# Kernel optimization log

Measured on AMD Instinct MI355X. Metric: run time of the kernel, lower is better.

## Reference

```python
import jax, jax.numpy as jnp
import numpy as np

U, I, D, L, NNZ, B = 100000, 50000, 64, 3, 3200000, 4096
N = U + I
MOMENTUM = 0.05

def setup_inputs() -> dict:
    key = jax.random.key(0)
    ks = jax.random.split(key, 10)
    return {
        'user_emb': jax.random.normal(ks[0], (U, D), jnp.float32) * 0.02,
        'item_emb': jax.random.normal(ks[1], (I, D), jnp.float32) * 0.02,
        'W': jax.random.normal(ks[2], (D, D), jnp.float32) * (1.0 / np.sqrt(D)),
        'b': jnp.zeros((D,), jnp.float32),
        'adj_rows': jax.random.randint(ks[3], (NNZ,), 0, N, jnp.int32),
        'adj_cols': jax.random.randint(ks[4], (NNZ,), 0, N, jnp.int32),
        'adj_vals': jax.random.uniform(ks[5], (NNZ,), jnp.float32) * 0.05,
        'users': jax.random.randint(ks[6], (B,), 0, U, jnp.int32),
        'items': jax.random.randint(ks[7], (B,), 0, I, jnp.int32),
        'u_his': jax.random.normal(ks[8], (U, D), jnp.float32),
        'i_his': jax.random.normal(ks[9], (I, D), jnp.float32),
    }

def _spmm(rows, cols, vals, x):
    # y = A @ x for sparse COO A: gather source rows, scale, scatter-add to dest rows
    return jax.ops.segment_sum(vals[:, None] * x[cols], rows, num_segments=N)

def reference(user_emb, item_emb, W, b, adj_rows, adj_cols, adj_vals, users, items, u_his, i_his):
    ego = jnp.concatenate([user_emb, item_emb], axis=0)  # [N, D]
    acc = ego
    cur = ego
    for _ in range(L):
        cur = _spmm(adj_rows, adj_cols, adj_vals, cur)
        acc = acc + cur
    all_emb = acc / (L + 1)           # mean over stacked layers
    u_all = all_emb[:U]
    i_all = all_emb[U:]
    u_online = u_all[users]           # [B, D]
    i_online = i_all[items]
    m = MOMENTUM
    u_target = jax.lax.stop_gradient(u_his[users] * m + u_online * (1.0 - m))
    i_target = jax.lax.stop_gradient(i_his[items] * m + i_online * (1.0 - m))
    p_u = u_online @ W.T + b
    p_i = i_online @ W.T + b
    return (p_u, u_target, p_i, i_target)
```

## Files before the change

### kernel.cpp

```cpp
#include <hip/hip_runtime.h>
#include <hip/hip_bf16.h>

#define U_CNT   100000
#define I_CNT   50000
#define D_DIM   64
#define N_NODES 150000
#define NNZ_E   3200000
#define B_SZ    4096

#define SUPER_SHIFT 12
#define NSUP 37
#define TILE1_E 4096
#define N_TILES1 ((NNZ_E + TILE1_E - 1) / TILE1_E)
#define TILE2_E 2048

#define CAP_SUP 98304
#define CAP2 4096
#define NSUB (NSUP * 32)
#define P2_BLOCKS_PER_SUP 24

#define CONV_THREADS (N_NODES * 16)
#define CONV_BLOCKS ((CONV_THREADS + 255) / 256)

typedef unsigned int uint;
typedef unsigned short ushort_t;
typedef _Float16 half_t;
typedef half_t half2_t __attribute__((ext_vector_type(2)));

union h2u_t { uint u; half2_t h; };
__device__ __forceinline__ half2_t u2h2(uint u) { h2u_t c; c.u = u; return c.h; }
__device__ __forceinline__ uint h22u(half2_t h) { h2u_t c; c.h = h; return c.u; }
__device__ __forceinline__ half2_t h2shfl_xor(half2_t v, int m) {
    h2u_t c; c.h = v; c.u = (uint)__shfl_xor((int)c.u, m, 64); return c.h;
}
__device__ __forceinline__ float h2lo(uint u) { return (float)u2h2(u)[0]; }
__device__ __forceinline__ float h2hi(uint u) { return (float)u2h2(u)[1]; }

__global__ __launch_bounds__(256) void init_cursors_kernel(int* __restrict__ scursor,
                                                           int* __restrict__ subcursor) {
    int i = blockIdx.x * 256 + threadIdx.x;
    if (i < NSUP) scursor[i] = i * CAP_SUP;
    if (i < NSUB) subcursor[i] = i * CAP2;
}

__global__ __launch_bounds__(256) void super_scatter_kernel(const int* __restrict__ rows,
                                                            const int* __restrict__ cols,
                                                            const float* __restrict__ vals,
                                                            int* __restrict__ scursor,
                                                            int2* __restrict__ smeta,
                                                            const float4* __restrict__ ue4,
                                                            const float4* __restrict__ ie4,
                                                            uint2* __restrict__ e2) {
    __shared__ int2 stage[TILE1_E];
    __shared__ int lcnt[NSUP];
    __shared__ int lbase[NSUP];
    __shared__ int gbase[NSUP];
    int tid = threadIdx.x;

    if (blockIdx.x >= N_TILES1) {
        int g = (blockIdx.x - N_TILES1) * 256 + tid;
        if (g < CONV_THREADS) {
            float4 f = (g < U_CNT * 16) ? ue4[g] : ie4[g - U_CNT * 16];
            half2_t a = { (half_t)f.x, (half_t)f.y };
            half2_t b = { (half_t)f.z, (half_t)f.w };
            uint2 o; o.x = h22u(a); o.y = h22u(b);
            e2[g] = o;
        }
        return;
    }

    int tile = blockIdx.x;
    int base = tile * TILE1_E;
    int cnt_tile = NNZ_E - base;
    if (cnt_tile > TILE1_E) cnt_tile = TILE1_E;

    if (tid < NSUP) lcnt[tid] = 0;
    __syncthreads();

    int nk = cnt_tile - tid;
    nk = (nk <= 0) ? 0 : (nk + 255) >> 8;

    int pk[16]; float vv[16]; int sp[16]; int rk[16];
    #pragma unroll
    for (int k = 0; k < 16; ++k) {
        if (k < nk) {
            int j = base + tid + (k << 8);
            int r = rows[j];
            int c = cols[j];
            vv[k] = vals[j];
            sp[k] = r >> SUPER_SHIFT;
            pk[k] = ((r & ((1 << SUPER_SHIFT) - 1)) << 18) | c;
            rk[k] = atomicAdd(&lcnt[sp[k]], 1);
        }
    }
    __syncthreads();

    if (tid < 64) {
        int c = (tid < NSUP) ? lcnt[tid] : 0;
        int incl = c;
        #pragma unroll
        for (int off = 1; off < 64; off <<= 1) {
            int t = __shfl_up(incl, off, 64);
            if (tid >= off) incl += t;
        }
        if (tid < NSUP) {
            lbase[tid] = incl - c;
            gbase[tid] = atomicAdd(&scursor[tid], c);
        }
    }
    __syncthreads();

    #pragma unroll
    for (int k = 0; k < 16; ++k) {
        if (k < nk) stage[lbase[sp[k]] + rk[k]] = make_int2(pk[k], __float_as_int(vv[k]));
    }
    __syncthreads();

    int wv = tid >> 6, ln = tid & 63;
    for (int s = wv; s < NSUP; s += 4) {
        int c = lcnt[s], lb = lbase[s], gb = gbase[s];
        int lim = (s + 1) * CAP_SUP;
        for (int t = ln; t < c; t += 64)
            if (gb + t < lim) smeta[gb + t] = stage[lb + t];
    }
}

__global__ __launch_bounds__(256) void sub_scatter_kernel(const int2* __restrict__ smeta,
                                                          const int* __restrict__ scursor,
                                                          int* __restrict__ subcursor,
                                                          int2* __restrict__ meta) {
    __shared__ int2 stage[TILE2_E];
    __shared__ int lcnt[32];
    __shared__ int lbase[32];
    __shared__ int gbase[32];
    int tid = threadIdx.x;
    int s    = blockIdx.x / P2_BLOCKS_PER_SUP;
    int slot = blockIdx.x % P2_BLOCKS_PER_SUP;
    int beg = s * CAP_SUP;
    int cnt_s = scursor[s] - beg;
    if (cnt_s > CAP_SUP) cnt_s = CAP_SUP;
    int end = beg + cnt_s;

    for (int tb = beg + slot * TILE2_E; tb < end; tb += P2_BLOCKS_PER_SUP * TILE2_E) {
        int cnt_tile = end - tb;
        if (cnt_tile > TILE2_E) cnt_tile = TILE2_E;

        if (tid < 32) lcnt[tid] = 0;
        __syncthreads();

        int nk = cnt_tile - tid;
        nk = (nk <= 0) ? 0 : (nk + 255) >> 8;

        int2 ed[8]; int sb[8]; int rk[8];
        #pragma unroll
        for (int k = 0; k < 8; ++k) {
            if (k < nk) {
                ed[k] = smeta[tb + tid + (k << 8)];
                sb[k] = ((uint)ed[k].x >> 25) & 31;
                rk[k] = atomicAdd(&lcnt[sb[k]], 1);
            }
        }
        __syncthreads();

        if (tid < 64) {
            int c = (tid < 32) ? lcnt[tid] : 0;
            int incl = c;
            #pragma unroll
            for (int off = 1; off < 32; off <<= 1) {
                int t = __shfl_up(incl, off, 64);
                if (tid >= off) incl += t;
            }
            if (tid < 32) {
                lbase[tid] = incl - c;
                gbase[tid] = atomicAdd(&subcursor[(s << 5) + tid], c);
            }
        }
        __syncthreads();

        #pragma unroll
        for (int k = 0; k < 8; ++k) {
            if (k < nk) stage[lbase[sb[k]] + rk[k]] = ed[k];
        }
        __syncthreads();

        int wv = tid >> 6, ln = tid & 63;
        for (int b = wv; b < 32; b += 4) {
            int c = lcnt[b], lb = lbase[b], gb = gbase[b];
            int lim = ((s << 5) + b + 1) * CAP2;
            for (int t = ln; t < c; t += 64)
                if (gb + t < lim) meta[gb + t] = stage[lb + t];
        }
        __syncthreads();
    }
}

__global__ __launch_bounds__(256) void row_sort_kernel(const int* __restrict__ subcursor,
                                                       int2* __restrict__ meta,
                                                       int* __restrict__ rstart,
                                                       int* __restrict__ rend) {
    __shared__ int2 stage[CAP2];
    __shared__ int rcnt[128];
    __shared__ int scan[128];
    __shared__ int cur[128];
    int g = blockIdx.x;
    int base = g * CAP2;
    int cnt = subcursor[g] - base;
    if (cnt > CAP2) cnt = CAP2;
    int tid = threadIdx.x;
    int s = g >> 5, q = g & 31;
    int r0 = (s << SUPER_SHIFT) + (q << 7);

    if (tid < 128) rcnt[tid] = 0;
    __syncthreads();

    for (int i = tid; i < cnt; i += 256) {
        int2 e = meta[base + i];
        stage[i] = e;
        atomicAdd(&rcnt[((uint)e.x >> 18) & 127], 1);
    }
    __syncthreads();

    if (tid < 128) scan[tid] = rcnt[tid];
    __syncthreads();
    for (int off = 1; off < 128; off <<= 1) {
        int t = (tid < 128 && tid >= off) ? scan[tid - off] : 0;
        __syncthreads();
        if (tid < 128) scan[tid] += t;
        __syncthreads();
    }
    if (tid < 128) {
        int excl = scan[tid] - rcnt[tid];
        cur[tid] = excl;
        int r = r0 + tid;
        if (r < N_NODES) {
            rstart[r] = base + excl;
            rend[r]   = base + scan[tid];
        }
    }
    __syncthreads();

    for (int i = tid; i < cnt; i += 256) {
        int2 e = stage[i];
        int rl = ((uint)e.x >> 18) & 127;
        int pos = atomicAdd(&cur[rl], 1);
        float v = __int_as_float(e.y);
        half2_t hv = { (half_t)v, (half_t)v };
        meta[base + pos] = make_int2(e.x & 0x3FFFF, (int)h22u(hv));
    }
}

__global__ __launch_bounds__(256) void spmm_fp16_kernel(const int* __restrict__ rstart,
                                                        const int* __restrict__ rend,
                                                        const int2* __restrict__ csr,
                                                        const ushort_t* __restrict__ x,
                                                        ushort_t* __restrict__ out) {
    int wid  = (blockIdx.x * blockDim.x + threadIdx.x) >> 6;
    int lane = threadIdx.x & 63;
    int sub  = lane >> 3;
    int l8   = lane & 7;
    if (wid >= N_NODES) return;
    int s = rstart[wid], e = rend[wid];
    const uint4* x4 = (const uint4*)x;

    int last = e - 1; if (last < s) last = s;
    auto ld = [&](int jj) -> int2 {
        int2 c = csr[jj < e ? jj : last];
        if (jj >= e) c.y = 0;
        return c;
    };

    half2_t a0 = { (half_t)0, (half_t)0 };
    half2_t a1 = a0, a2 = a0, a3 = a0;

    int j = s + sub;
    int2 c0 = ld(j);
    int2 c1 = ld(j + 8);
    int2 c2 = ld(j + 16);
    int2 c3 = ld(j + 24);
    for (; j < e; j += 32) {
        uint4 x0 = x4[(size_t)(c0.x & 0x3FFFF) * 8 + l8];
        uint4 x1 = x4[(size_t)(c1.x & 0x3FFFF) * 8 + l8];
        uint4 x2 = x4[(size_t)(c2.x & 0x3FFFF) * 8 + l8];
        uint4 x3 = x4[(size_t)(c3.x & 0x3FFFF) * 8 + l8];
        int jn = j + 32;
        int2 n0 = ld(jn);
        int2 n1 = ld(jn + 8);
        int2 n2 = ld(jn + 16);
        int2 n3 = ld(jn + 24);
        half2_t v0 = u2h2((uint)c0.y);
        a0 += u2h2(x0.x) * v0; a1 += u2h2(x0.y) * v0;
        a2 += u2h2(x0.z) * v0; a3 += u2h2(x0.w) * v0;
        half2_t v1 = u2h2((uint)c1.y);
        a0 += u2h2(x1.x) * v1; a1 += u2h2(x1.y) * v1;
        a2 += u2h2(x1.z) * v1; a3 += u2h2(x1.w) * v1;
        half2_t v2 = u2h2((uint)c2.y);
        a0 += u2h2(x2.x) * v2; a1 += u2h2(x2.y) * v2;
        a2 += u2h2(x2.z) * v2; a3 += u2h2(x2.w) * v2;
        half2_t v3 = u2h2((uint)c3.y);
        a0 += u2h2(x3.x) * v3; a1 += u2h2(x3.y) * v3;
        a2 += u2h2(x3.z) * v3; a3 += u2h2(x3.w) * v3;
        c0 = n0; c1 = n1; c2 = n2; c3 = n3;
    }
    a0 += h2shfl_xor(a0, 8);  a1 += h2shfl_xor(a1, 8);
    a2 += h2shfl_xor(a2, 8);  a3 += h2shfl_xor(a3, 8);
    a0 += h2shfl_xor(a0, 16); a1 += h2shfl_xor(a1, 16);
    a2 += h2shfl_xor(a2, 16); a3 += h2shfl_xor(a3, 16);
    a0 += h2shfl_xor(a0, 32); a1 += h2shfl_xor(a1, 32);
    a2 += h2shfl_xor(a2, 32); a3 += h2shfl_xor(a3, 32);

    if (sub == 0) {
        uint4 r;
        r.x = h22u(a0); r.y = h22u(a1); r.z = h22u(a2); r.w = h22u(a3);
        ((uint4*)out)[(size_t)wid * 8 + l8] = r;
    }
}

__global__ __launch_bounds__(256) void epilogue_kernel(const int* __restrict__ users,
                                                       const int* __restrict__ items,
                                                       const int* __restrict__ rstart,
                                                       const int* __restrict__ rend,
                                                       const int2* __restrict__ csr,
                                                       const ushort_t* __restrict__ ebuf,
                                                       const ushort_t* __restrict__ buf1,
                                                       const ushort_t* __restrict__ buf2,
                                                       const float* __restrict__ u_his,
                                                       const float* __restrict__ i_his,
                                                       const float* __restrict__ W,
                                                       const float* __restrict__ bvec,
                                                       float* __restrict__ out) {
    __shared__ float Wt[D_DIM * 65];
    __shared__ float bsh[D_DIM];
    __shared__ float on_s[4][D_DIM];
    for (int t = threadIdx.x; t < D_DIM * D_DIM; t += blockDim.x) {
        int j = t >> 6, k = t & 63;
        Wt[k * 65 + j] = W[t];
    }
    if (threadIdx.x < D_DIM) bsh[threadIdx.x] = bvec[threadIdx.x];

    int wv   = threadIdx.x >> 6;
    int wid  = blockIdx.x * 4 + wv;
    int lane = threadIdx.x & 63;
    int sub  = lane >> 4;
    int l16  = lane & 15;

    bool is_user = (wid < B_SZ);
    int  samp = is_user ? wid : wid - B_SZ;
    int  idx  = is_user ? users[samp] : items[samp];
    int  row  = is_user ? idx : (U_CNT + idx);

    const float* his = is_user ? u_his : i_his;
    float hisv = his[(size_t)idx * D_DIM + lane];
    uint2 eg = make_uint2(0, 0), b1v = eg, b2v = eg;
    if (sub == 0) {
        eg  = ((const uint2*)ebuf)[(size_t)row * 16 + l16];
        b1v = ((const uint2*)buf1)[(size_t)row * 16 + l16];
        b2v = ((const uint2*)buf2)[(size_t)row * 16 + l16];
    }

    int s = rstart[row], e = rend[row];
    int last = e - 1; if (last < s) last = s;
    auto ld = [&](int jj) -> int2 {
        int2 c = csr[jj < e ? jj : last];
        if (jj >= e) c.y = 0;
        return c;
    };
    half2_t c0 = { (half_t)0, (half_t)0 };
    half2_t c1 = c0;
    int j = s + sub;
    int2 e0 = ld(j);
    int2 e1 = ld(j + 4);
    int2 e2 = ld(j + 8);
    int2 e3 = ld(j + 12);
    for (; j < e; j += 16) {
        uint2 x0 = ((const uint2*)buf2)[(size_t)(e0.x & 0x3FFFF) * 16 + l16];
        uint2 x1 = ((const uint2*)buf2)[(size_t)(e1.x & 0x3FFFF) * 16 + l16];
        uint2 x2 = ((const uint2*)buf2)[(size_t)(e2.x & 0x3FFFF) * 16 + l16];
        uint2 x3 = ((const uint2*)buf2)[(size_t)(e3.x & 0x3FFFF) * 16 + l16];
        int jn = j + 16;
        int2 n0 = ld(jn);
        int2 n1 = ld(jn + 4);
        int2 n2 = ld(jn + 8);
        int2 n3 = ld(jn + 12);
        half2_t v0 = u2h2((uint)e0.y);
        c0 += u2h2(x0.x) * v0; c1 += u2h2(x0.y) * v0;
        half2_t v1 = u2h2((uint)e1.y);
        c0 += u2h2(x1.x) * v1; c1 += u2h2(x1.y) * v1;
        half2_t v2 = u2h2((uint)e2.y);
        c0 += u2h2(x2.x) * v2; c1 += u2h2(x2.y) * v2;
        half2_t v3 = u2h2((uint)e3.y);
        c0 += u2h2(x3.x) * v3; c1 += u2h2(x3.y) * v3;
        e0 = n0; e1 = n1; e2 = n2; e3 = n3;
    }
    c0 += h2shfl_xor(c0, 16); c1 += h2shfl_xor(c1, 16);
    c0 += h2shfl_xor(c0, 32); c1 += h2shfl_xor(c1, 32);

    if (sub == 0) {
        on_s[wv][l16 * 4 + 0] = (h2lo(eg.x) + h2lo(b1v.x) + h2lo(b2v.x) + (float)c0[0]) * 0.25f;
        on_s[wv][l16 * 4 + 1] = (h2hi(eg.x) + h2hi(b1v.x) + h2hi(b2v.x) + (float)c0[1]) * 0.25f;
        on_s[wv][l16 * 4 + 2] = (h2lo(eg.y) + h2lo(b1v.y) + h2lo(b2v.y) + (float)c1[0]) * 0.25f;
        on_s[wv][l16 * 4 + 3] = (h2hi(eg.y) + h2hi(b1v.y) + h2hi(b2v.y) + (float)c1[1]) * 0.25f;
    }
    __syncthreads();

    float online = on_s[wv][lane];
    float target = 0.05f * hisv + 0.95f * online;

    float p = bsh[lane];
    #pragma unroll
    for (int k = 0; k < D_DIM; ++k) {
        float ok = __shfl(online, k, 64);
        p = fmaf(ok, Wt[k * 65 + lane], p);
    }

    size_t base = is_user ? 0 : (size_t)2 * B_SZ * D_DIM;
    out[base + (size_t)samp * D_DIM + lane] = p;
    out[base + (size_t)B_SZ * D_DIM + (size_t)samp * D_DIM + lane] = target;
}


extern "C" void kernel_launch(void* const* d_in, const int* in_sizes, int n_in,
                              void* d_out, int out_size, void* d_ws, size_t ws_size,
                              hipStream_t stream) {
    const float* user_emb = (const float*)d_in[0];
    const float* item_emb = (const float*)d_in[1];
    const float* W        = (const float*)d_in[2];
    const float* bvec     = (const float*)d_in[3];
    const int*   adj_rows = (const int*)d_in[4];
    const int*   adj_cols = (const int*)d_in[5];
    const float* adj_vals = (const float*)d_in[6];
    const int*   users    = (const int*)d_in[7];
    const int*   items    = (const int*)d_in[8];
    const float* u_his    = (const float*)d_in[9];
    const float* i_his    = (const float*)d_in[10];
    float* out = (float*)d_out;

    char* ws = (char*)d_ws;
    size_t o = 0;
    ushort_t* ebuf  = (ushort_t*)(ws + o); o += (size_t)N_NODES * D_DIM * 2;
    ushort_t* buf1  = (ushort_t*)(ws + o); o += (size_t)N_NODES * D_DIM * 2;
    int2*  smeta    = (int2*)(ws + o);     o += (size_t)NSUP * CAP_SUP * 8;
    int2*  meta     = (int2*)(ws + o);     o += (size_t)NSUB * CAP2 * 8;
    int*   rstart   = (int*)(ws + o);      o += (size_t)N_NODES * 4;
    int*   rend     = (int*)(ws + o);      o += (size_t)N_NODES * 4;
    int*   scursor  = (int*)(ws + o);      o += 64 * 4;
    int*   subcursor= (int*)(ws + o);      o += (size_t)NSUB * 4;
    ushort_t* buf2  = (ushort_t*)smeta;
    (void)ws_size; (void)o; (void)in_sizes; (void)n_in; (void)out_size;

    init_cursors_kernel<<<(NSUB + 255) / 256, 256, 0, stream>>>(scursor, subcursor);
    super_scatter_kernel<<<N_TILES1 + CONV_BLOCKS, 256, 0, stream>>>(
        adj_rows, adj_cols, adj_vals, scursor, smeta,
        (const float4*)user_emb, (const float4*)item_emb, (uint2*)ebuf);
    sub_scatter_kernel<<<NSUP * P2_BLOCKS_PER_SUP, 256, 0, stream>>>(smeta, scursor,
                                                                     subcursor, meta);
    row_sort_kernel<<<NSUB, 256, 0, stream>>>(subcursor, meta, rstart, rend);

    int spmm_blocks = (N_NODES + 3) / 4;
    spmm_fp16_kernel<<<spmm_blocks, 256, 0, stream>>>(rstart, rend, meta, ebuf, buf1);
    spmm_fp16_kernel<<<spmm_blocks, 256, 0, stream>>>(rstart, rend, meta, buf1, buf2);

    epilogue_kernel<<<(2 * B_SZ) / 4, 256, 0, stream>>>(users, items, rstart, rend, meta,
                                                        ebuf, buf1, buf2,
                                                        u_his, i_his, W, bvec, out);
}
```

Before: 332.7 us.

## Fuse row sort into first SpMM layer and stage CSR segments in shared memory

Merges the per-bucket row sort with the first SpMM pass. Each 512-thread block sorts its 128-row bucket in registers and shared memory, using a wave shuffle scan, then computes those rows directly from the LDS-staged edge list. The second layer reloads the bucket's edges into LDS and reuses them the same way. This removes one kernel launch and the global re-read of the CSR metadata. In exchange, each block now handles a fixed 128 rows with 8 waves of 16 rows each, so rows with many edges can leave the load unbalanced, and there are far fewer blocks than before (1184 versus 37500).

New measurement: 328.7 us. About the same (-1.2%).

```diff
diff --git a/kernel.cpp b/kernel.cpp
--- a/kernel.cpp
+++ b/kernel.cpp
@@ -194,124 +194,142 @@
     }
 }
 
-__global__ __launch_bounds__(256) void row_sort_kernel(const int* __restrict__ subcursor,
-                                                       int2* __restrict__ meta,
-                                                       int* __restrict__ rstart,
-                                                       int* __restrict__ rend) {
+template<int SORT>
+__global__ __launch_bounds__(512) void sort_spmm_kernel(const int* __restrict__ subcursor,
+                                                        int2* __restrict__ meta,
+                                                        int* __restrict__ rstart,
+                                                        int* __restrict__ rend,
+                                                        const ushort_t* __restrict__ x,
+                                                        ushort_t* __restrict__ out) {
     __shared__ int2 stage[CAP2];
     __shared__ int rcnt[128];
-    __shared__ int scan[128];
-    __shared__ int cur[128];
+    __shared__ int rs[128];
+    __shared__ int re_[128];
     int g = blockIdx.x;
     int base = g * CAP2;
     int cnt = subcursor[g] - base;
     if (cnt > CAP2) cnt = CAP2;
     int tid = threadIdx.x;
-    int s = g >> 5, q = g & 31;
-    int r0 = (s << SUPER_SHIFT) + (q << 7);
-
-    if (tid < 128) rcnt[tid] = 0;
-    __syncthreads();
-
-    for (int i = tid; i < cnt; i += 256) {
-        int2 e = meta[base + i];
-        stage[i] = e;
-        atomicAdd(&rcnt[((uint)e.x >> 18) & 127], 1);
-    }
-    __syncthreads();
-
-    if (tid < 128) scan[tid] = rcnt[tid];
-    __syncthreads();
-    for (int off = 1; off < 128; off <<= 1) {
-        int t = (tid < 128 && tid >= off) ? scan[tid - off] : 0;
-        __syncthreads();
-        if (tid < 128) scan[tid] += t;
-        __syncthreads();
-    }
-    if (tid < 128) {
-        int excl = scan[tid] - rcnt[tid];
-        cur[tid] = excl;
-        int r = r0 + tid;
-        if (r < N_NODES) {
-            rstart[r] = base + excl;
-            rend[r]   = base + scan[tid];
-        }
-    }
-    __syncthreads();
-
-    for (int i = tid; i < cnt; i += 256) {
-        int2 e = stage[i];
-        int rl = ((uint)e.x >> 18) & 127;
-        int pos = atomicAdd(&cur[rl], 1);
-        float v = __int_as_float(e.y);
-        half2_t hv = { (half_t)v, (half_t)v };
-        meta[base + pos] = make_int2(e.x & 0x3FFFF, (int)h22u(hv));
-    }
-}
-
-__global__ __launch_bounds__(256) void spmm_fp16_kernel(const int* __restrict__ rstart,
-                                                        const int* __restrict__ rend,
-                                                        const int2* __restrict__ csr,
-                                                        const ushort_t* __restrict__ x,
-                                                        ushort_t* __restrict__ out) {
-    int wid  = (blockIdx.x * blockDim.x + threadIdx.x) >> 6;
-    int lane = threadIdx.x & 63;
+    int r0 = ((g >> 5) << SUPER_SHIFT) + ((g & 31) << 7);
+
+    if (SORT) {
+        if (tid < 128) rcnt[tid] = 0;
+        __syncthreads();
+
+        int2 ek[8]; int rk[8];
+        int nk = cnt - tid;
+        nk = (nk <= 0) ? 0 : (nk + 511) >> 9;
+        #pragma unroll
+        for (int k = 0; k < 8; ++k) {
+            if (k < nk) {
+                ek[k] = meta[base + tid + (k << 9)];
+                rk[k] = atomicAdd(&rcnt[((uint)ek[k].x >> 18) & 127], 1);
+            }
+        }
+        __syncthreads();
+
+        if (tid < 64) {
+            int c0 = rcnt[2 * tid], c1 = rcnt[2 * tid + 1];
+            int s2 = c0 + c1, incl = s2;
+            #pragma unroll
+            for (int off = 1; off < 64; off <<= 1) {
+                int t = __shfl_up(incl, off, 64);
+                if (tid >= off) incl += t;
+            }
+            int s0 = incl - s2, s1 = incl - c1;
+            rs[2 * tid] = s0;      re_[2 * tid] = s0 + c0;
+            rs[2 * tid + 1] = s1;  re_[2 * tid + 1] = incl;
+            int r = r0 + 2 * tid;
+            if (r < N_NODES)     { rstart[r]     = base + s0; rend[r]     = base + s0 + c0; }
+            if (r + 1 < N_NODES) { rstart[r + 1] = base + s1; rend[r + 1] = base + incl;    }
+        }
+        __syncthreads();
+
+        #pragma unroll
+        for (int k = 0; k < 8; ++k) {
+            if (k < nk) {
+                int rl = ((uint)ek[k].x >> 18) & 127;
+                int pos = rs[rl] + rk[k];
+                float v = __int_as_float(ek[k].y);
+                half2_t hv = { (half_t)v, (half_t)v };
+                int2 f = make_int2(ek[k].x & 0x3FFFF, (int)h22u(hv));
+                stage[pos] = f;
+                meta[base + pos] = f;
+            }
+        }
+        __syncthreads();
+    } else {
+        for (int i = tid; i < cnt; i += 512) stage[i] = meta[base + i];
+        if (tid < 128) {
+            int r = r0 + tid;
+            if (r < N_NODES) { rs[tid] = rstart[r] - base; re_[tid] = rend[r] - base; }
+            else             { rs[tid] = 0; re_[tid] = 0; }
+        }
+        __syncthreads();
+    }
+
+    int wv   = tid >> 6;
+    int lane = tid & 63;
     int sub  = lane >> 3;
     int l8   = lane & 7;
-    if (wid >= N_NODES) return;
-    int s = rstart[wid], e = rend[wid];
     const uint4* x4 = (const uint4*)x;
 
-    int last = e - 1; if (last < s) last = s;
-    auto ld = [&](int jj) -> int2 {
-        int2 c = csr[jj < e ? jj : last];
-        if (jj >= e) c.y = 0;
-        return c;
-    };
-
-    half2_t a0 = { (half_t)0, (half_t)0 };
-    half2_t a1 = a0, a2 = a0, a3 = a0;
-
-    int j = s + sub;
-    int2 c0 = ld(j);
-    int2 c1 = ld(j + 8);
-    int2 c2 = ld(j + 16);
-    int2 c3 = ld(j + 24);
-    for (; j < e; j += 32) {
-        uint4 x0 = x4[(size_t)(c0.x & 0x3FFFF) * 8 + l8];
-        uint4 x1 = x4[(size_t)(c1.x & 0x3FFFF) * 8 + l8];
-        uint4 x2 = x4[(size_t)(c2.x & 0x3FFFF) * 8 + l8];
-        uint4 x3 = x4[(size_t)(c3.x & 0x3FFFF) * 8 + l8];
-        int jn = j + 32;
-        int2 n0 = ld(jn);
-        int2 n1 = ld(jn + 8);
-        int2 n2 = ld(jn + 16);
-        int2 n3 = ld(jn + 24);
-        half2_t v0 = u2h2((uint)c0.y);
-        a0 += u2h2(x0.x) * v0; a1 += u2h2(x0.y) * v0;
-        a2 += u2h2(x0.z) * v0; a3 += u2h2(x0.w) * v0;
-        half2_t v1 = u2h2((uint)c1.y);
-        a0 += u2h2(x1.x) * v1; a1 += u2h2(x1.y) * v1;
-        a2 += u2h2(x1.z) * v1; a3 += u2h2(x1.w) * v1;
-        half2_t v2 = u2h2((uint)c2.y);
-        a0 += u2h2(x2.x) * v2; a1 += u2h2(x2.y) * v2;
-        a2 += u2h2(x2.z) * v2; a3 += u2h2(x2.w) * v2;
-        half2_t v3 = u2h2((uint)c3.y);
-        a0 += u2h2(x3.x) * v3; a1 += u2h2(x3.y) * v3;
-        a2 += u2h2(x3.z) * v3; a3 += u2h2(x3.w) * v3;
-        c0 = n0; c1 = n1; c2 = n2; c3 = n3;
-    }
-    a0 += h2shfl_xor(a0, 8);  a1 += h2shfl_xor(a1, 8);
-    a2 += h2shfl_xor(a2, 8);  a3 += h2shfl_xor(a3, 8);
-    a0 += h2shfl_xor(a0, 16); a1 += h2shfl_xor(a1, 16);
-    a2 += h2shfl_xor(a2, 16); a3 += h2shfl_xor(a3, 16);
-    a0 += h2shfl_xor(a0, 32); a1 += h2shfl_xor(a1, 32);
-    a2 += h2shfl_xor(a2, 32); a3 += h2shfl_xor(a3, 32);
-
-    if (sub == 0) {
-        uint4 r;
-        r.x = h22u(a0); r.y = h22u(a1); r.z = h22u(a2); r.w = h22u(a3);
-        ((uint4*)out)[(size_t)wid * 8 + l8] = r;
+    for (int rr = 0; rr < 16; ++rr) {
+        int rl = (wv << 4) + rr;
+        int s = rs[rl], e = re_[rl];
+        half2_t a0 = { (half_t)0, (half_t)0 };
+        half2_t a1 = a0, a2 = a0, a3 = a0;
+
+        if (e > s) {
+            int last = e - 1;
+            auto ldl = [&](int jj) -> int2 {
+                int2 c = stage[jj < e ? jj : last];
+                if (jj >= e) c.y = 0;
+                return c;
+            };
+            int j = s + sub;
+            int2 c0 = ldl(j);
+            int2 c1 = ldl(j + 8);
+            int2 c2 = ldl(j + 16);
+            int2 c3 = ldl(j + 24);
+            for (; j < e; j += 32) {
+                uint4 x0 = x4[(size_t)(c0.x & 0x3FFFF) * 8 + l8];
+                uint4 x1 = x4[(size_t)(c1.x & 0x3FFFF) * 8 + l8];
+                uint4 x2 = x4[(size_t)(c2.x & 0x3FFFF) * 8 + l8];
+                uint4 x3 = x4[(size_t)(c3.x & 0x3FFFF) * 8 + l8];
+                int jn = j + 32;
+                int2 n0 = ldl(jn);
+                int2 n1 = ldl(jn + 8);
+                int2 n2 = ldl(jn + 16);
+                int2 n3 = ldl(jn + 24);
+                half2_t v0 = u2h2((uint)c0.y);
+                a0 += u2h2(x0.x) * v0; a1 += u2h2(x0.y) * v0;
+                a2 += u2h2(x0.z) * v0; a3 += u2h2(x0.w) * v0;
+                half2_t v1 = u2h2((uint)c1.y);
+                a0 += u2h2(x1.x) * v1; a1 += u2h2(x1.y) * v1;
+                a2 += u2h2(x1.z) * v1; a3 += u2h2(x1.w) * v1;
+                half2_t v2 = u2h2((uint)c2.y);
+                a0 += u2h2(x2.x) * v2; a1 += u2h2(x2.y) * v2;
+                a2 += u2h2(x2.z) * v2; a3 += u2h2(x2.w) * v2;
+                half2_t v3 = u2h2((uint)c3.y);
+                a0 += u2h2(x3.x) * v3; a1 += u2h2(x3.y) * v3;
+                a2 += u2h2(x3.z) * v3; a3 += u2h2(x3.w) * v3;
+                c0 = n0; c1 = n1; c2 = n2; c3 = n3;
+            }
+        }
+        a0 += h2shfl_xor(a0, 8);  a1 += h2shfl_xor(a1, 8);
+        a2 += h2shfl_xor(a2, 8);  a3 += h2shfl_xor(a3, 8);
+        a0 += h2shfl_xor(a0, 16); a1 += h2shfl_xor(a1, 16);
+        a2 += h2shfl_xor(a2, 16); a3 += h2shfl_xor(a3, 16);
+        a0 += h2shfl_xor(a0, 32); a1 += h2shfl_xor(a1, 32);
+        a2 += h2shfl_xor(a2, 32); a3 += h2shfl_xor(a3, 32);
+
+        int wid = r0 + rl;
+        if (sub == 0 && wid < N_NODES) {
+            uint4 r;
+            r.x = h22u(a0); r.y = h22u(a1); r.z = h22u(a2); r.w = h22u(a3);
+            ((uint4*)out)[(size_t)wid * 8 + l8] = r;
+        }
     }
 }
 
@@ -453,11 +471,11 @@
         (const float4*)user_emb, (const float4*)item_emb, (uint2*)ebuf);
     sub_scatter_kernel<<<NSUP * P2_BLOCKS_PER_SUP, 256, 0, stream>>>(smeta, scursor,
                                                                      subcursor, meta);
-    row_sort_kernel<<<NSUB, 256, 0, stream>>>(subcursor, meta, rstart, rend);
-
-    int spmm_blocks = (N_NODES + 3) / 4;
-    spmm_fp16_kernel<<<spmm_blocks, 256, 0, stream>>>(rstart, rend, meta, ebuf, buf1);
-    spmm_fp16_kernel<<<spmm_blocks, 256, 0, stream>>>(rstart, rend, meta, buf1, buf2);
+
+    sort_spmm_kernel<1><<<NSUB, 512, 0, stream>>>(subcursor, meta, rstart, rend,
+                                                  ebuf, buf1);
+    sort_spmm_kernel<0><<<NSUB, 512, 0, stream>>>(subcursor, meta, rstart, rend,
+                                                  buf1, buf2);
 
     epilogue_kernel<<<(2 * B_SZ) / 4, 256, 0, stream>>>(users, items, rstart, rend, meta,
                                                         ebuf, buf1, buf2,
```

## Replace multi-pass bucket sort with direct per-row atomic slot scatter

Applied to the files above, without the earlier changes.

Drops the three-stage COO-to-CSR build (super-bucket scatter, sub-bucket scatter, per-row counting sort) in favour of one scatter kernel. That kernel reserves a slot in a fixed-capacity ELL-like region per destination row (56 slots) with a global atomicAdd and writes the column and fp16 value there. The SpMM and epilogue kernels then read each row from its fixed offset using the per-row cursor as its end. This removes two kernel launches and several full passes over the edge list. In exchange it relies on about 3.2M global atomics spread over 150k counters, uses a larger padded metadata buffer, and silently drops edges for any row with more than 56 entries. Edge order within a row is also no longer deterministic, so fp16 summation order can vary between runs.

Measured after the change: 490.8 us. +47.5%, slower.

```diff
diff --git a/kernel.cpp b/kernel.cpp
--- a/kernel.cpp
+++ b/kernel.cpp
@@ -8,16 +8,10 @@
 #define NNZ_E   3200000
 #define B_SZ    4096
 
-#define SUPER_SHIFT 12
-#define NSUP 37
 #define TILE1_E 4096
 #define N_TILES1 ((NNZ_E + TILE1_E - 1) / TILE1_E)
-#define TILE2_E 2048
-
-#define CAP_SUP 98304
-#define CAP2 4096
-#define NSUB (NSUP * 32)
-#define P2_BLOCKS_PER_SUP 24
+
+#define CAP_ROW 56
 
 #define CONV_THREADS (N_NODES * 16)
 #define CONV_BLOCKS ((CONV_THREADS + 255) / 256)
@@ -36,25 +30,19 @@
 __device__ __forceinline__ float h2lo(uint u) { return (float)u2h2(u)[0]; }
 __device__ __forceinline__ float h2hi(uint u) { return (float)u2h2(u)[1]; }
 
-__global__ __launch_bounds__(256) void init_cursors_kernel(int* __restrict__ scursor,
-                                                           int* __restrict__ subcursor) {
+__global__ __launch_bounds__(256) void init_rowcur_kernel(int* __restrict__ rowcur) {
     int i = blockIdx.x * 256 + threadIdx.x;
-    if (i < NSUP) scursor[i] = i * CAP_SUP;
-    if (i < NSUB) subcursor[i] = i * CAP2;
-}
-
-__global__ __launch_bounds__(256) void super_scatter_kernel(const int* __restrict__ rows,
-                                                            const int* __restrict__ cols,
-                                                            const float* __restrict__ vals,
-                                                            int* __restrict__ scursor,
-                                                            int2* __restrict__ smeta,
-                                                            const float4* __restrict__ ue4,
-                                                            const float4* __restrict__ ie4,
-                                                            uint2* __restrict__ e2) {
-    __shared__ int2 stage[TILE1_E];
-    __shared__ int lcnt[NSUP];
-    __shared__ int lbase[NSUP];
-    __shared__ int gbase[NSUP];
+    if (i < N_NODES) rowcur[i] = i * CAP_ROW;
+}
+
+__global__ __launch_bounds__(256) void scatter_kernel(const int* __restrict__ rows,
+                                                      const int* __restrict__ cols,
+                                                      const float* __restrict__ vals,
+                                                      int* __restrict__ rowcur,
+                                                      int2* __restrict__ meta,
+                                                      const float4* __restrict__ ue4,
+                                                      const float4* __restrict__ ie4,
+                                                      uint2* __restrict__ e2) {
     int tid = threadIdx.x;
 
     if (blockIdx.x >= N_TILES1) {
@@ -69,188 +57,37 @@
         return;
     }
 
-    int tile = blockIdx.x;
-    int base = tile * TILE1_E;
-    int cnt_tile = NNZ_E - base;
-    if (cnt_tile > TILE1_E) cnt_tile = TILE1_E;
-
-    if (tid < NSUP) lcnt[tid] = 0;
-    __syncthreads();
-
-    int nk = cnt_tile - tid;
+    int base = blockIdx.x * TILE1_E;
+    int nk = NNZ_E - base - tid;
     nk = (nk <= 0) ? 0 : (nk + 255) >> 8;
 
-    int pk[16]; float vv[16]; int sp[16]; int rk[16];
+    int rr[16]; int cc[16]; float vv[16];
     #pragma unroll
     for (int k = 0; k < 16; ++k) {
         if (k < nk) {
             int j = base + tid + (k << 8);
-            int r = rows[j];
-            int c = cols[j];
+            rr[k] = rows[j];
+            cc[k] = cols[j];
             vv[k] = vals[j];
-            sp[k] = r >> SUPER_SHIFT;
-            pk[k] = ((r & ((1 << SUPER_SHIFT) - 1)) << 18) | c;
-            rk[k] = atomicAdd(&lcnt[sp[k]], 1);
-        }
-    }
-    __syncthreads();
-
-    if (tid < 64) {
-        int c = (tid < NSUP) ? lcnt[tid] : 0;
-        int incl = c;
-        #pragma unroll
-        for (int off = 1; off < 64; off <<= 1) {
-            int t = __shfl_up(incl, off, 64);
-            if (tid >= off) incl += t;
-        }
-        if (tid < NSUP) {
-            lbase[tid] = incl - c;
-            gbase[tid] = atomicAdd(&scursor[tid], c);
-        }
-    }
-    __syncthreads();
-
+        }
+    }
+    int pos[16];
     #pragma unroll
     for (int k = 0; k < 16; ++k) {
-        if (k < nk) stage[lbase[sp[k]] + rk[k]] = make_int2(pk[k], __float_as_int(vv[k]));
-    }
-    __syncthreads();
-
-    int wv = tid >> 6, ln = tid & 63;
-    for (int s = wv; s < NSUP; s += 4) {
-        int c = lcnt[s], lb = lbase[s], gb = gbase[s];
-        int lim = (s + 1) * CAP_SUP;
-        for (int t = ln; t < c; t += 64)
-            if (gb + t < lim) smeta[gb + t] = stage[lb + t];
-    }
-}
-
-__global__ __launch_bounds__(256) void sub_scatter_kernel(const int2* __restrict__ smeta,
-                                                          const int* __restrict__ scursor,
-                                                          int* __restrict__ subcursor,
-                                                          int2* __restrict__ meta) {
-    __shared__ int2 stage[TILE2_E];
-    __shared__ int lcnt[32];
-    __shared__ int lbase[32];
-    __shared__ int gbase[32];
-    int tid = threadIdx.x;
-    int s    = blockIdx.x / P2_BLOCKS_PER_SUP;
-    int slot = blockIdx.x % P2_BLOCKS_PER_SUP;
-    int beg = s * CAP_SUP;
-    int cnt_s = scursor[s] - beg;
-    if (cnt_s > CAP_SUP) cnt_s = CAP_SUP;
-    int end = beg + cnt_s;
-
-    for (int tb = beg + slot * TILE2_E; tb < end; tb += P2_BLOCKS_PER_SUP * TILE2_E) {
-        int cnt_tile = end - tb;
-        if (cnt_tile > TILE2_E) cnt_tile = TILE2_E;
-
-        if (tid < 32) lcnt[tid] = 0;
-        __syncthreads();
-
-        int nk = cnt_tile - tid;
-        nk = (nk <= 0) ? 0 : (nk + 255) >> 8;
-
-        int2 ed[8]; int sb[8]; int rk[8];
-        #pragma unroll
-        for (int k = 0; k < 8; ++k) {
-            if (k < nk) {
-                ed[k] = smeta[tb + tid + (k << 8)];
-                sb[k] = ((uint)ed[k].x >> 25) & 31;
-                rk[k] = atomicAdd(&lcnt[sb[k]], 1);
+        if (k < nk) pos[k] = atomicAdd(&rowcur[rr[k]], 1);
+    }
+    #pragma unroll
+    for (int k = 0; k < 16; ++k) {
+        if (k < nk) {
+            if (pos[k] < rr[k] * CAP_ROW + CAP_ROW) {
+                half2_t hv = { (half_t)vv[k], (half_t)vv[k] };
+                meta[pos[k]] = make_int2(cc[k], (int)h22u(hv));
             }
         }
-        __syncthreads();
-
-        if (tid < 64) {
-            int c = (tid < 32) ? lcnt[tid] : 0;
-            int incl = c;
-            #pragma unroll
-            for (int off = 1; off < 32; off <<= 1) {
-                int t = __shfl_up(incl, off, 64);
-                if (tid >= off) incl += t;
-            }
-            if (tid < 32) {
-                lbase[tid] = incl - c;
-                gbase[tid] = atomicAdd(&subcursor[(s << 5) + tid], c);
-            }
-        }
-        __syncthreads();
-
-        #pragma unroll
-        for (int k = 0; k < 8; ++k) {
-            if (k < nk) stage[lbase[sb[k]] + rk[k]] = ed[k];
-        }
-        __syncthreads();
-
-        int wv = tid >> 6, ln = tid & 63;
-        for (int b = wv; b < 32; b += 4) {
-            int c = lcnt[b], lb = lbase[b], gb = gbase[b];
-            int lim = ((s << 5) + b + 1) * CAP2;
-            for (int t = ln; t < c; t += 64)
-                if (gb + t < lim) meta[gb + t] = stage[lb + t];
-        }
-        __syncthreads();
-    }
-}
-
-__global__ __launch_bounds__(256) void row_sort_kernel(const int* __restrict__ subcursor,
-                                                       int2* __restrict__ meta,
-                                                       int* __restrict__ rstart,
-                                                       int* __restrict__ rend) {
-    __shared__ int2 stage[CAP2];
-    __shared__ int rcnt[128];
-    __shared__ int scan[128];
-    __shared__ int cur[128];
-    int g = blockIdx.x;
-    int base = g * CAP2;
-    int cnt = subcursor[g] - base;
-    if (cnt > CAP2) cnt = CAP2;
-    int tid = threadIdx.x;
-    int s = g >> 5, q = g & 31;
-    int r0 = (s << SUPER_SHIFT) + (q << 7);
-
-    if (tid < 128) rcnt[tid] = 0;
-    __syncthreads();
-
-    for (int i = tid; i < cnt; i += 256) {
-        int2 e = meta[base + i];
-        stage[i] = e;
-        atomicAdd(&rcnt[((uint)e.x >> 18) & 127], 1);
-    }
-    __syncthreads();
-
-    if (tid < 128) scan[tid] = rcnt[tid];
-    __syncthreads();
-    for (int off = 1; off < 128; off <<= 1) {
-        int t = (tid < 128 && tid >= off) ? scan[tid - off] : 0;
-        __syncthreads();
-        if (tid < 128) scan[tid] += t;
-        __syncthreads();
-    }
-    if (tid < 128) {
-        int excl = scan[tid] - rcnt[tid];
-        cur[tid] = excl;
-        int r = r0 + tid;
-        if (r < N_NODES) {
-            rstart[r] = base + excl;
-            rend[r]   = base + scan[tid];
-        }
-    }
-    __syncthreads();
-
-    for (int i = tid; i < cnt; i += 256) {
-        int2 e = stage[i];
-        int rl = ((uint)e.x >> 18) & 127;
-        int pos = atomicAdd(&cur[rl], 1);
-        float v = __int_as_float(e.y);
-        half2_t hv = { (half_t)v, (half_t)v };
-        meta[base + pos] = make_int2(e.x & 0x3FFFF, (int)h22u(hv));
-    }
-}
-
-__global__ __launch_bounds__(256) void spmm_fp16_kernel(const int* __restrict__ rstart,
-                                                        const int* __restrict__ rend,
+    }
+}
+
+__global__ __launch_bounds__(256) void spmm_fp16_kernel(const int* __restrict__ rowcur,
                                                         const int2* __restrict__ csr,
                                                         const ushort_t* __restrict__ x,
                                                         ushort_t* __restrict__ out) {
@@ -259,47 +96,50 @@
     int sub  = lane >> 3;
     int l8   = lane & 7;
     if (wid >= N_NODES) return;
-    int s = rstart[wid], e = rend[wid];
+    int s = wid * CAP_ROW;
+    int e = rowcur[wid];
+    int cap = s + CAP_ROW; if (e > cap) e = cap;
     const uint4* x4 = (const uint4*)x;
-
-    int last = e - 1; if (last < s) last = s;
-    auto ld = [&](int jj) -> int2 {
-        int2 c = csr[jj < e ? jj : last];
-        if (jj >= e) c.y = 0;
-        return c;
-    };
 
     half2_t a0 = { (half_t)0, (half_t)0 };
     half2_t a1 = a0, a2 = a0, a3 = a0;
 
-    int j = s + sub;
-    int2 c0 = ld(j);
-    int2 c1 = ld(j + 8);
-    int2 c2 = ld(j + 16);
-    int2 c3 = ld(j + 24);
-    for (; j < e; j += 32) {
-        uint4 x0 = x4[(size_t)(c0.x & 0x3FFFF) * 8 + l8];
-        uint4 x1 = x4[(size_t)(c1.x & 0x3FFFF) * 8 + l8];
-        uint4 x2 = x4[(size_t)(c2.x & 0x3FFFF) * 8 + l8];
-        uint4 x3 = x4[(size_t)(c3.x & 0x3FFFF) * 8 + l8];
-        int jn = j + 32;
-        int2 n0 = ld(jn);
-        int2 n1 = ld(jn + 8);
-        int2 n2 = ld(jn + 16);
-        int2 n3 = ld(jn + 24);
-        half2_t v0 = u2h2((uint)c0.y);
-        a0 += u2h2(x0.x) * v0; a1 += u2h2(x0.y) * v0;
-        a2 += u2h2(x0.z) * v0; a3 += u2h2(x0.w) * v0;
-        half2_t v1 = u2h2((uint)c1.y);
-        a0 += u2h2(x1.x) * v1; a1 += u2h2(x1.y) * v1;
-        a2 += u2h2(x1.z) * v1; a3 += u2h2(x1.w) * v1;
-        half2_t v2 = u2h2((uint)c2.y);
-        a0 += u2h2(x2.x) * v2; a1 += u2h2(x2.y) * v2;
-        a2 += u2h2(x2.z) * v2; a3 += u2h2(x2.w) * v2;
-        half2_t v3 = u2h2((uint)c3.y);
-        a0 += u2h2(x3.x) * v3; a1 += u2h2(x3.y) * v3;
-        a2 += u2h2(x3.z) * v3; a3 += u2h2(x3.w) * v3;
-        c0 = n0; c1 = n1; c2 = n2; c3 = n3;
+    if (e > s) {
+        int last = e - 1;
+        auto ld = [&](int jj) -> int2 {
+            int2 c = csr[jj < e ? jj : last];
+            if (jj >= e) c.y = 0;
+            return c;
+        };
+        int j = s + sub;
+        int2 c0 = ld(j);
+        int2 c1 = ld(j + 8);
+        int2 c2 = ld(j + 16);
+        int2 c3 = ld(j + 24);
+        for (; j < e; j += 32) {
+            uint4 x0 = x4[(size_t)c0.x * 8 + l8];
+            uint4 x1 = x4[(size_t)c1.x * 8 + l8];
+            uint4 x2 = x4[(size_t)c2.x * 8 + l8];
+            uint4 x3 = x4[(size_t)c3.x * 8 + l8];
+            int jn = j + 32;
+            int2 n0 = ld(jn);
+            int2 n1 = ld(jn + 8);
+            int2 n2 = ld(jn + 16);
+            int2 n3 = ld(jn + 24);
+            half2_t v0 = u2h2((uint)c0.y);
+            a0 += u2h2(x0.x) * v0; a1 += u2h2(x0.y) * v0;
+            a2 += u2h2(x0.z) * v0; a3 += u2h2(x0.w) * v0;
+            half2_t v1 = u2h2((uint)c1.y);
+            a0 += u2h2(x1.x) * v1; a1 += u2h2(x1.y) * v1;
+            a2 += u2h2(x1.z) * v1; a3 += u2h2(x1.w) * v1;
+            half2_t v2 = u2h2((uint)c2.y);
+            a0 += u2h2(x2.x) * v2; a1 += u2h2(x2.y) * v2;
+            a2 += u2h2(x2.z) * v2; a3 += u2h2(x2.w) * v2;
+            half2_t v3 = u2h2((uint)c3.y);
+            a0 += u2h2(x3.x) * v3; a1 += u2h2(x3.y) * v3;
+            a2 += u2h2(x3.z) * v3; a3 += u2h2(x3.w) * v3;
+            c0 = n0; c1 = n1; c2 = n2; c3 = n3;
+        }
     }
     a0 += h2shfl_xor(a0, 8);  a1 += h2shfl_xor(a1, 8);
     a2 += h2shfl_xor(a2, 8);  a3 += h2shfl_xor(a3, 8);
@@ -317,8 +157,7 @@
 
 __global__ __launch_bounds__(256) void epilogue_kernel(const int* __restrict__ users,
                                                        const int* __restrict__ items,
-                                                       const int* __restrict__ rstart,
-                                                       const int* __restrict__ rend,
+                                                       const int* __restrict__ rowcur,
                                                        const int2* __restrict__ csr,
                                                        const ushort_t* __restrict__ ebuf,
                                                        const ushort_t* __restrict__ buf1,
@@ -357,39 +196,43 @@
         b2v = ((const uint2*)buf2)[(size_t)row * 16 + l16];
     }
 
-    int s = rstart[row], e = rend[row];
-    int last = e - 1; if (last < s) last = s;
-    auto ld = [&](int jj) -> int2 {
-        int2 c = csr[jj < e ? jj : last];
-        if (jj >= e) c.y = 0;
-        return c;
-    };
+    int s = row * CAP_ROW;
+    int e = rowcur[row];
+    int cap = s + CAP_ROW; if (e > cap) e = cap;
     half2_t c0 = { (half_t)0, (half_t)0 };
     half2_t c1 = c0;
-    int j = s + sub;
-    int2 e0 = ld(j);
-    int2 e1 = ld(j + 4);
-    int2 e2 = ld(j + 8);
-    int2 e3 = ld(j + 12);
-    for (; j < e; j += 16) {
-        uint2 x0 = ((const uint2*)buf2)[(size_t)(e0.x & 0x3FFFF) * 16 + l16];
-        uint2 x1 = ((const uint2*)buf2)[(size_t)(e1.x & 0x3FFFF) * 16 + l16];
-        uint2 x2 = ((const uint2*)buf2)[(size_t)(e2.x & 0x3FFFF) * 16 + l16];
-        uint2 x3 = ((const uint2*)buf2)[(size_t)(e3.x & 0x3FFFF) * 16 + l16];
-        int jn = j + 16;
-        int2 n0 = ld(jn);
-        int2 n1 = ld(jn + 4);
-        int2 n2 = ld(jn + 8);
-        int2 n3 = ld(jn + 12);
-        half2_t v0 = u2h2((uint)e0.y);
-        c0 += u2h2(x0.x) * v0; c1 += u2h2(x0.y) * v0;
-        half2_t v1 = u2h2((uint)e1.y);
-        c0 += u2h2(x1.x) * v1; c1 += u2h2(x1.y) * v1;
-        half2_t v2 = u2h2((uint)e2.y);
-        c0 += u2h2(x2.x) * v2; c1 += u2h2(x2.y) * v2;
-        half2_t v3 = u2h2((uint)e3.y);
-        c0 += u2h2(x3.x) * v3; c1 += u2h2(x3.y) * v3;
-        e0 = n0; e1 = n1; e2 = n2; e3 = n3;
+    if (e > s) {
+        int last = e - 1;
+        auto ld = [&](int jj) -> int2 {
+            int2 c = csr[jj < e ? jj : last];
+            if (jj >= e) c.y = 0;
+            return c;
+        };
+        int j = s + sub;
+        int2 e0 = ld(j);
+        int2 e1 = ld(j + 4);
+        int2 e2 = ld(j + 8);
+        int2 e3 = ld(j + 12);
+        for (; j < e; j += 16) {
+            uint2 x0 = ((const uint2*)buf2)[(size_t)e0.x * 16 + l16];
+            uint2 x1 = ((const uint2*)buf2)[(size_t)e1.x * 16 + l16];
+            uint2 x2 = ((const uint2*)buf2)[(size_t)e2.x * 16 + l16];
+            uint2 x3 = ((const uint2*)buf2)[(size_t)e3.x * 16 + l16];
+            int jn = j + 16;
+            int2 n0 = ld(jn);
+            int2 n1 = ld(jn + 4);
+            int2 n2 = ld(jn + 8);
+            int2 n3 = ld(jn + 12);
+            half2_t v0 = u2h2((uint)e0.y);
+            c0 += u2h2(x0.x) * v0; c1 += u2h2(x0.y) * v0;
+            half2_t v1 = u2h2((uint)e1.y);
+            c0 += u2h2(x1.x) * v1; c1 += u2h2(x1.y) * v1;
+            half2_t v2 = u2h2((uint)e2.y);
+            c0 += u2h2(x2.x) * v2; c1 += u2h2(x2.y) * v2;
+            half2_t v3 = u2h2((uint)e3.y);
+            c0 += u2h2(x3.x) * v3; c1 += u2h2(x3.y) * v3;
+            e0 = n0; e1 = n1; e2 = n2; e3 = n3;
+        }
     }
     c0 += h2shfl_xor(c0, 16); c1 += h2shfl_xor(c1, 16);
     c0 += h2shfl_xor(c0, 32); c1 += h2shfl_xor(c1, 32);
@@ -438,28 +281,21 @@
     size_t o = 0;
     ushort_t* ebuf  = (ushort_t*)(ws + o); o += (size_t)N_NODES * D_DIM * 2;
     ushort_t* buf1  = (ushort_t*)(ws + o); o += (size_t)N_NODES * D_DIM * 2;
-    int2*  smeta    = (int2*)(ws + o);     o += (size_t)NSUP * CAP_SUP * 8;
-    int2*  meta     = (int2*)(ws + o);     o += (size_t)NSUB * CAP2 * 8;
-    int*   rstart   = (int*)(ws + o);      o += (size_t)N_NODES * 4;
-    int*   rend     = (int*)(ws + o);      o += (size_t)N_NODES * 4;
-    int*   scursor  = (int*)(ws + o);      o += 64 * 4;
-    int*   subcursor= (int*)(ws + o);      o += (size_t)NSUB * 4;
-    ushort_t* buf2  = (ushort_t*)smeta;
+    ushort_t* buf2  = (ushort_t*)(ws + o); o += (size_t)N_NODES * D_DIM * 2;
+    int2*  meta     = (int2*)(ws + o);     o += (size_t)N_NODES * CAP_ROW * 8;
+    int*   rowcur   = (int*)(ws + o);      o += (size_t)N_NODES * 4;
     (void)ws_size; (void)o; (void)in_sizes; (void)n_in; (void)out_size;
 
-    init_cursors_kernel<<<(NSUB + 255) / 256, 256, 0, stream>>>(scursor, subcursor);
-    super_scatter_kernel<<<N_TILES1 + CONV_BLOCKS, 256, 0, stream>>>(
-        adj_rows, adj_cols, adj_vals, scursor, smeta,
+    init_rowcur_kernel<<<(N_NODES + 255) / 256, 256, 0, stream>>>(rowcur);
+    scatter_kernel<<<N_TILES1 + CONV_BLOCKS, 256, 0, stream>>>(
+        adj_rows, adj_cols, adj_vals, rowcur, meta,
         (const float4*)user_emb, (const float4*)item_emb, (uint2*)ebuf);
-    sub_scatter_kernel<<<NSUP * P2_BLOCKS_PER_SUP, 256, 0, stream>>>(smeta, scursor,
-                                                                     subcursor, meta);
-    row_sort_kernel<<<NSUB, 256, 0, stream>>>(subcursor, meta, rstart, rend);
 
     int spmm_blocks = (N_NODES + 3) / 4;
-    spmm_fp16_kernel<<<spmm_blocks, 256, 0, stream>>>(rstart, rend, meta, ebuf, buf1);
-    spmm_fp16_kernel<<<spmm_blocks, 256, 0, stream>>>(rstart, rend, meta, buf1, buf2);
-
-    epilogue_kernel<<<(2 * B_SZ) / 4, 256, 0, stream>>>(users, items, rstart, rend, meta,
+    spmm_fp16_kernel<<<spmm_blocks, 256, 0, stream>>>(rowcur, meta, ebuf, buf1);
+    spmm_fp16_kernel<<<spmm_blocks, 256, 0, stream>>>(rowcur, meta, buf1, buf2);
+
+    epilogue_kernel<<<(2 * B_SZ) / 4, 256, 0, stream>>>(users, items, rowcur, meta,
                                                         ebuf, buf1, buf2,
                                                         u_his, i_his, W, bvec, out);
 }
```

## Replace two-pass bucket scatter with single-pass direct scatter to 128-row buckets

Applied to the files above, without the earlier changes.

Merges the super-bucket and sub-bucket scatter passes into one kernel that bins each edge straight into one of 1172 fine row buckets. It uses per-block shared-memory histograms and global cursor atomics, then writes directly to the bucket. This drops an intermediate pass and its full read and write of the edge array, plus one kernel launch. In exchange, global writes are no longer staged and coalesced per bucket, so they become scattered, and each block issues up to 1172 global atomics. The conversion blocks now handle four elements per thread, and buf2 gets its own workspace slot.

After: 335.0 us. No clear change (+0.7%).

```diff
diff --git a/kernel.cpp b/kernel.cpp
--- a/kernel.cpp
+++ b/kernel.cpp
@@ -8,19 +8,14 @@
 #define NNZ_E   3200000
 #define B_SZ    4096
 
-#define SUPER_SHIFT 12
-#define NSUP 37
-#define TILE1_E 4096
-#define N_TILES1 ((NNZ_E + TILE1_E - 1) / TILE1_E)
-#define TILE2_E 2048
-
-#define CAP_SUP 98304
+#define NSUB 1172
 #define CAP2 4096
-#define NSUB (NSUP * 32)
-#define P2_BLOCKS_PER_SUP 24
+#define TILE_E 8192
+#define N_TILES ((NNZ_E + TILE_E - 1) / TILE_E)
 
 #define CONV_THREADS (N_NODES * 16)
-#define CONV_BLOCKS ((CONV_THREADS + 255) / 256)
+#define CONV_PER_BLK (512 * 4)
+#define CONV_BLOCKS ((CONV_THREADS + CONV_PER_BLK - 1) / CONV_PER_BLK)
 
 typedef unsigned int uint;
 typedef unsigned short ushort_t;
@@ -36,161 +31,75 @@
 __device__ __forceinline__ float h2lo(uint u) { return (float)u2h2(u)[0]; }
 __device__ __forceinline__ float h2hi(uint u) { return (float)u2h2(u)[1]; }
 
-__global__ __launch_bounds__(256) void init_cursors_kernel(int* __restrict__ scursor,
-                                                           int* __restrict__ subcursor) {
+__global__ __launch_bounds__(256) void init_cursors_kernel(int* __restrict__ subcursor) {
     int i = blockIdx.x * 256 + threadIdx.x;
-    if (i < NSUP) scursor[i] = i * CAP_SUP;
     if (i < NSUB) subcursor[i] = i * CAP2;
 }
 
-__global__ __launch_bounds__(256) void super_scatter_kernel(const int* __restrict__ rows,
-                                                            const int* __restrict__ cols,
-                                                            const float* __restrict__ vals,
-                                                            int* __restrict__ scursor,
-                                                            int2* __restrict__ smeta,
-                                                            const float4* __restrict__ ue4,
-                                                            const float4* __restrict__ ie4,
-                                                            uint2* __restrict__ e2) {
-    __shared__ int2 stage[TILE1_E];
-    __shared__ int lcnt[NSUP];
-    __shared__ int lbase[NSUP];
-    __shared__ int gbase[NSUP];
+__global__ __launch_bounds__(512) void scatter_kernel(const int* __restrict__ rows,
+                                                      const int* __restrict__ cols,
+                                                      const float* __restrict__ vals,
+                                                      int* __restrict__ subcursor,
+                                                      int2* __restrict__ meta,
+                                                      const float4* __restrict__ ue4,
+                                                      const float4* __restrict__ ie4,
+                                                      uint2* __restrict__ e2) {
     int tid = threadIdx.x;
 
-    if (blockIdx.x >= N_TILES1) {
-        int g = (blockIdx.x - N_TILES1) * 256 + tid;
-        if (g < CONV_THREADS) {
-            float4 f = (g < U_CNT * 16) ? ue4[g] : ie4[g - U_CNT * 16];
-            half2_t a = { (half_t)f.x, (half_t)f.y };
-            half2_t b = { (half_t)f.z, (half_t)f.w };
-            uint2 o; o.x = h22u(a); o.y = h22u(b);
-            e2[g] = o;
+    if (blockIdx.x >= N_TILES) {
+        int g0 = (blockIdx.x - N_TILES) * CONV_PER_BLK + tid;
+        #pragma unroll
+        for (int k = 0; k < 4; ++k) {
+            int g = g0 + k * 512;
+            if (g < CONV_THREADS) {
+                float4 f = (g < U_CNT * 16) ? ue4[g] : ie4[g - U_CNT * 16];
+                half2_t a = { (half_t)f.x, (half_t)f.y };
+                half2_t b = { (half_t)f.z, (half_t)f.w };
+                uint2 o; o.x = h22u(a); o.y = h22u(b);
+                e2[g] = o;
+            }
         }
         return;
     }
 
-    int tile = blockIdx.x;
-    int base = tile * TILE1_E;
-    int cnt_tile = NNZ_E - base;
-    if (cnt_tile > TILE1_E) cnt_tile = TILE1_E;
-
-    if (tid < NSUP) lcnt[tid] = 0;
-    __syncthreads();
-
-    int nk = cnt_tile - tid;
-    nk = (nk <= 0) ? 0 : (nk + 255) >> 8;
-
-    int pk[16]; float vv[16]; int sp[16]; int rk[16];
+    __shared__ int lcnt[NSUB];
+    __shared__ int gbase[NSUB];
+
+    for (int i = tid; i < NSUB; i += 512) lcnt[i] = 0;
+    __syncthreads();
+
+    int base = blockIdx.x * TILE_E;
+    int nk = NNZ_E - base - tid;
+    nk = (nk <= 0) ? 0 : (nk + 511) >> 9;
+
+    int pk[16]; float vv[16]; int sb[16]; int rk[16];
     #pragma unroll
     for (int k = 0; k < 16; ++k) {
         if (k < nk) {
-            int j = base + tid + (k << 8);
+            int j = base + tid + (k << 9);
             int r = rows[j];
             int c = cols[j];
             vv[k] = vals[j];
-            sp[k] = r >> SUPER_SHIFT;
-            pk[k] = ((r & ((1 << SUPER_SHIFT) - 1)) << 18) | c;
-            rk[k] = atomicAdd(&lcnt[sp[k]], 1);
+            sb[k] = r >> 7;
+            pk[k] = ((r & 127) << 18) | c;
+            rk[k] = atomicAdd(&lcnt[sb[k]], 1);
         }
     }
     __syncthreads();
 
-    if (tid < 64) {
-        int c = (tid < NSUP) ? lcnt[tid] : 0;
-        int incl = c;
-        #pragma unroll
-        for (int off = 1; off < 64; off <<= 1) {
-            int t = __shfl_up(incl, off, 64);
-            if (tid >= off) incl += t;
-        }
-        if (tid < NSUP) {
-            lbase[tid] = incl - c;
-            gbase[tid] = atomicAdd(&scursor[tid], c);
-        }
+    for (int i = tid; i < NSUB; i += 512) {
+        int c = lcnt[i];
+        gbase[i] = (c > 0) ? atomicAdd(&subcursor[i], c) : 0;
     }
     __syncthreads();
 
     #pragma unroll
     for (int k = 0; k < 16; ++k) {
-        if (k < nk) stage[lbase[sp[k]] + rk[k]] = make_int2(pk[k], __float_as_int(vv[k]));
-    }
-    __syncthreads();
-
-    int wv = tid >> 6, ln = tid & 63;
-    for (int s = wv; s < NSUP; s += 4) {
-        int c = lcnt[s], lb = lbase[s], gb = gbase[s];
-        int lim = (s + 1) * CAP_SUP;
-        for (int t = ln; t < c; t += 64)
-            if (gb + t < lim) smeta[gb + t] = stage[lb + t];
-    }
-}
-
-__global__ __launch_bounds__(256) void sub_scatter_kernel(const int2* __restrict__ smeta,
-                                                          const int* __restrict__ scursor,
-                                                          int* __restrict__ subcursor,
-                                                          int2* __restrict__ meta) {
-    __shared__ int2 stage[TILE2_E];
-    __shared__ int lcnt[32];
-    __shared__ int lbase[32];
-    __shared__ int gbase[32];
-    int tid = threadIdx.x;
-    int s    = blockIdx.x / P2_BLOCKS_PER_SUP;
-    int slot = blockIdx.x % P2_BLOCKS_PER_SUP;
-    int beg = s * CAP_SUP;
-    int cnt_s = scursor[s] - beg;
-    if (cnt_s > CAP_SUP) cnt_s = CAP_SUP;
-    int end = beg + cnt_s;
-
-    for (int tb = beg + slot * TILE2_E; tb < end; tb += P2_BLOCKS_PER_SUP * TILE2_E) {
-        int cnt_tile = end - tb;
-        if (cnt_tile > TILE2_E) cnt_tile = TILE2_E;
-
-        if (tid < 32) lcnt[tid] = 0;
-        __syncthreads();
-
-        int nk = cnt_tile - tid;
-        nk = (nk <= 0) ? 0 : (nk + 255) >> 8;
-
-        int2 ed[8]; int sb[8]; int rk[8];
-        #pragma unroll
-        for (int k = 0; k < 8; ++k) {
-            if (k < nk) {
-                ed[k] = smeta[tb + tid + (k << 8)];
-                sb[k] = ((uint)ed[k].x >> 25) & 31;
-                rk[k] = atomicAdd(&lcnt[sb[k]], 1);
-            }
+        if (k < nk) {
+            int pos = gbase[sb[k]] + rk[k];
+            if (pos < (sb[k] + 1) * CAP2)
+                meta[pos] = make_int2(pk[k], __float_as_int(vv[k]));
         }
-        __syncthreads();
-
-        if (tid < 64) {
-            int c = (tid < 32) ? lcnt[tid] : 0;
-            int incl = c;
-            #pragma unroll
-            for (int off = 1; off < 32; off <<= 1) {
-                int t = __shfl_up(incl, off, 64);
-                if (tid >= off) incl += t;
-            }
-            if (tid < 32) {
-                lbase[tid] = incl - c;
-                gbase[tid] = atomicAdd(&subcursor[(s << 5) + tid], c);
-            }
-        }
-        __syncthreads();
-
-        #pragma unroll
-        for (int k = 0; k < 8; ++k) {
-            if (k < nk) stage[lbase[sb[k]] + rk[k]] = ed[k];
-        }
-        __syncthreads();
-
-        int wv = tid >> 6, ln = tid & 63;
-        for (int b = wv; b < 32; b += 4) {
-            int c = lcnt[b], lb = lbase[b], gb = gbase[b];
-            int lim = ((s << 5) + b + 1) * CAP2;
-            for (int t = ln; t < c; t += 64)
-                if (gb + t < lim) meta[gb + t] = stage[lb + t];
-        }
-        __syncthreads();
     }
 }
 
@@ -207,8 +116,7 @@
     int cnt = subcursor[g] - base;
     if (cnt > CAP2) cnt = CAP2;
     int tid = threadIdx.x;
-    int s = g >> 5, q = g & 31;
-    int r0 = (s << SUPER_SHIFT) + (q << 7);
+    int r0 = g << 7;
 
     if (tid < 128) rcnt[tid] = 0;
     __syncthreads();
@@ -438,21 +346,17 @@
     size_t o = 0;
     ushort_t* ebuf  = (ushort_t*)(ws + o); o += (size_t)N_NODES * D_DIM * 2;
     ushort_t* buf1  = (ushort_t*)(ws + o); o += (size_t)N_NODES * D_DIM * 2;
-    int2*  smeta    = (int2*)(ws + o);     o += (size_t)NSUP * CAP_SUP * 8;
+    ushort_t* buf2  = (ushort_t*)(ws + o); o += (size_t)N_NODES * D_DIM * 2;
     int2*  meta     = (int2*)(ws + o);     o += (size_t)NSUB * CAP2 * 8;
     int*   rstart   = (int*)(ws + o);      o += (size_t)N_NODES * 4;
     int*   rend     = (int*)(ws + o);      o += (size_t)N_NODES * 4;
-    int*   scursor  = (int*)(ws + o);      o += 64 * 4;
     int*   subcursor= (int*)(ws + o);      o += (size_t)NSUB * 4;
-    ushort_t* buf2  = (ushort_t*)smeta;
     (void)ws_size; (void)o; (void)in_sizes; (void)n_in; (void)out_size;
 
-    init_cursors_kernel<<<(NSUB + 255) / 256, 256, 0, stream>>>(scursor, subcursor);
-    super_scatter_kernel<<<N_TILES1 + CONV_BLOCKS, 256, 0, stream>>>(
-        adj_rows, adj_cols, adj_vals, scursor, smeta,
+    init_cursors_kernel<<<(NSUB + 255) / 256, 256, 0, stream>>>(subcursor);
+    scatter_kernel<<<N_TILES + CONV_BLOCKS, 512, 0, stream>>>(
+        adj_rows, adj_cols, adj_vals, subcursor, meta,
         (const float4*)user_emb, (const float4*)item_emb, (uint2*)ebuf);
-    sub_scatter_kernel<<<NSUP * P2_BLOCKS_PER_SUP, 256, 0, stream>>>(smeta, scursor,
-                                                                     subcursor, meta);
     row_sort_kernel<<<NSUB, 256, 0, stream>>>(subcursor, meta, rstart, rend);
 
     int spmm_blocks = (N_NODES + 3) / 4;
```
